# Kernel tuning notes

Hardware: AMD Instinct MI355X
Metric: run time of the kernel (lower is better)

Reference implementation:

```python
import jax, jax.numpy as jnp
import numpy as np

D_MODEL = 1024
L_MAX = 2048
BATCH = 4
ORDER = 2
FILTER_ORDER = 64
EMB_DIM = 3            # HyenaFilter default positional-embedding dim
SHORT_K = 3
HEAD_DIM = D_MODEL     # num_heads = 1
TOTAL_WIDTH = D_MODEL * (ORDER + 1)
# ExponentialModulation constants (Safari defaults)
MAX_DECAY = np.log(1e-2) / 0.3
MIN_DECAY = np.log(1e-2) / 1.5


def setup_inputs() -> dict:
    key = jax.random.key(0)
    ks = jax.random.split(key, 12)
    s = 0.02
    return {
        "u": jax.random.normal(ks[0], (BATCH, L_MAX, D_MODEL), jnp.float32),
        "in_w": jax.random.normal(ks[1], (D_MODEL, TOTAL_WIDTH), jnp.float32) * s,
        "in_b": jnp.zeros((TOTAL_WIDTH,), jnp.float32),
        "short_w": jax.random.normal(ks[2], (TOTAL_WIDTH, 1, SHORT_K), jnp.float32) * 0.3,
        "short_b": jnp.zeros((TOTAL_WIDTH,), jnp.float32),
        "mlp_w0": jax.random.normal(ks[3], (EMB_DIM, FILTER_ORDER), jnp.float32) * 0.4,
        "mlp_b0": jnp.zeros((FILTER_ORDER,), jnp.float32),
        "freq0": 10.0 * jnp.ones((1, FILTER_ORDER), jnp.float32),
        "mlp_w1": jax.random.normal(ks[4], (FILTER_ORDER, FILTER_ORDER), jnp.float32) * 0.12,
        "mlp_b1": jnp.zeros((FILTER_ORDER,), jnp.float32),
        "freq1": 10.0 * jnp.ones((1, FILTER_ORDER), jnp.float32),
        "mlp_w2": jax.random.normal(ks[5], (FILTER_ORDER, FILTER_ORDER), jnp.float32) * 0.12,
        "mlp_b2": jnp.zeros((FILTER_ORDER,), jnp.float32),
        "freq2": 10.0 * jnp.ones((1, FILTER_ORDER), jnp.float32),
        "mlp_w3": jax.random.normal(ks[6], (FILTER_ORDER, HEAD_DIM), jnp.float32) * 0.1,
        "filter_bias": jax.random.normal(ks[7], (HEAD_DIM,), jnp.float32),
        "out_w": jax.random.normal(ks[8], (D_MODEL, D_MODEL), jnp.float32) * s,
        "out_b": jnp.zeros((D_MODEL,), jnp.float32),
    }


def _pos_emb(L):
    # PositionalEmbedding: t in [0,1], plus exp(-1j * f * w) real/imag bands
    bands = (EMB_DIM - 1) // 2
    t = jnp.linspace(0.0, 1.0, L, dtype=jnp.float32)[:, None]                # (L, 1)
    w = 2.0 * jnp.pi * jnp.linspace(0.0, L - 1.0, L, dtype=jnp.float32)[:, None] / L
    f = jnp.linspace(1e-4, float(bands - 1), bands, dtype=jnp.float32)[None, :]
    phase = f * w                                                             # (L, bands)
    # exp(-1j*phase): real = cos(phase), imag = -sin(phase)
    z = jnp.concatenate([t, jnp.cos(phase), -jnp.sin(phase)], axis=-1)        # (L, EMB_DIM)
    return z, t


def _implicit_filter(L, mlp_w0, mlp_b0, freq0, mlp_w1, mlp_b1, freq1,
                     mlp_w2, mlp_b2, freq2, mlp_w3):
    z, t = _pos_emb(L)
    h = jnp.sin(freq0 * (z @ mlp_w0 + mlp_b0))
    h = jnp.sin(freq1 * (h @ mlp_w1 + mlp_b1))
    h = jnp.sin(freq2 * (h @ mlp_w2 + mlp_b2))
    h = h @ mlp_w3                                                            # (L, HEAD_DIM)
    # ExponentialModulation (shift = 0)
    deltas = jnp.linspace(MIN_DECAY, MAX_DECAY, HEAD_DIM, dtype=jnp.float32)[None, :]
    h = h * jnp.exp(-t * jnp.abs(deltas))
    return h                                                                  # (L, HEAD_DIM)


def _fftconv(u, k, bias):
    # u: (b, v, L), k: (v, L), bias: (v,) -- causal linear conv via 2L FFT
    L = u.shape[-1]
    n = 2 * L
    k_f = jnp.fft.rfft(k, n=n) / n                                            # (v, n//2+1)
    u_f = jnp.fft.rfft(u, n=n)                                                # (b, v, n//2+1)
    y = jnp.fft.irfft(u_f * k_f, n=n, norm="forward")[..., :L]
    return y + u * bias[:, None]


def reference(u, in_w, in_b, short_w, short_b,
              mlp_w0, mlp_b0, freq0, mlp_w1, mlp_b1, freq1,
              mlp_w2, mlp_b2, freq2, mlp_w3, filter_bias, out_w, out_b):
    b, l, d = u.shape
    up = u @ in_w + in_b                                                      # (b, l, 3d)
    up = jnp.transpose(up, (0, 2, 1))                                         # (b, 3d, l)
    # depthwise causal short conv (torch pad=k-1 both sides then [:l] == left pad only)
    uc = jax.lax.conv_general_dilated(
        up, short_w, window_strides=(1,), padding=[(SHORT_K - 1, 0)],
        dimension_numbers=("NCH", "OIH", "NCH"), feature_group_count=TOTAL_WIDTH)
    uc = uc + short_b[None, :, None]                                          # (b, 3d, l)
    x0, x1, v = jnp.split(uc, ORDER + 1, axis=1)                              # each (b, d, l)
    k = _implicit_filter(l, mlp_w0, mlp_b0, freq0, mlp_w1, mlp_b1, freq1,
                         mlp_w2, mlp_b2, freq2, mlp_w3).T                     # (d, l)
    v = v * x1                                                                # gate
    v = _fftconv(v, k, filter_bias)                                           # long conv
    y = jnp.transpose(v * x0, (0, 2, 1))                                      # (b, l, d)
    return y @ out_w + out_b
```

## Files before the change

kernel.cpp:

```cpp
#include <hip/hip_runtime.h>
#include <stdint.h>

typedef unsigned short u16;
typedef __attribute__((ext_vector_type(8))) short short8;
typedef __attribute__((ext_vector_type(4))) short short4x;
typedef __attribute__((ext_vector_type(4))) float f32x4;

#define PI_F 3.14159265358979323846f
#define L_SEQ 2048
#define NFFT 4096
#define DM 1024
#define TW 3072
#define BATCH 4

__device__ __forceinline__ u16 f2bf(float f){
  union { float f; uint32_t u; } v; v.f = f;
  uint32_t r = v.u + 0x7fffu + ((v.u >> 16) & 1u);
  return (u16)(r >> 16);
}
__device__ __forceinline__ float bf2f(u16 h){
  union { uint32_t u; float f; } v; v.u = ((uint32_t)h) << 16;
  return v.f;
}

__device__ __forceinline__ void async16(const void* g, void* l){
  __builtin_amdgcn_global_load_lds(
      (const __attribute__((address_space(1))) void*)g,
      (__attribute__((address_space(3))) void*)l, 16, 0, 0);
}

__device__ __forceinline__ void sincos_rev(float rev, float& sn, float& cs){
  asm("v_sin_f32 %0, %1" : "=v"(sn) : "v"(rev));
  asm("v_cos_f32 %0, %1" : "=v"(cs) : "v"(rev));
}

__device__ __forceinline__ float2 cmulf(float2 a, float c, float s){
  return make_float2(a.x*c - a.y*s, a.x*s + a.y*c);
}

__device__ __forceinline__ int P16(int i){ return i + (i >> 4); }

__device__ static constexpr int BR4[16] = {0,8,4,12,2,10,6,14,1,9,5,13,3,11,7,15};

template<int SGN>
__device__ __forceinline__ void fft16(float2* a){
  const float s = (float)SGN;
  static constexpr float tc[8]  = {1.f, 0.92387953f, 0.70710678f, 0.38268343f,
                                   0.f, -0.38268343f, -0.70710678f, -0.92387953f};
  static constexpr float ts_[8] = {0.f, -0.38268343f, -0.70710678f, -0.92387953f,
                                   -1.f, -0.92387953f, -0.70710678f, -0.38268343f};
  #pragma unroll
  for (int j = 0; j < 8; ++j){
    float2 u = a[j], v = a[j+8];
    float2 d = make_float2(u.x - v.x, u.y - v.y);
    a[j] = make_float2(u.x + v.x, u.y + v.y);
    a[j+8] = cmulf(d, tc[j], s*ts_[j]);
  }
  #pragma unroll
  for (int g = 0; g < 2; ++g){
    int b = g*8;
    #pragma unroll
    for (int j = 0; j < 4; ++j){
      float2 u = a[b+j], v = a[b+j+4];
      float2 d = make_float2(u.x - v.x, u.y - v.y);
      a[b+j] = make_float2(u.x + v.x, u.y + v.y);
      a[b+j+4] = cmulf(d, tc[2*j], s*ts_[2*j]);
    }
  }
  #pragma unroll
  for (int g = 0; g < 4; ++g){
    int b = g*4;
    #pragma unroll
    for (int j = 0; j < 2; ++j){
      float2 u = a[b+j], v = a[b+j+2];
      float2 d = make_float2(u.x - v.x, u.y - v.y);
      a[b+j] = make_float2(u.x + v.x, u.y + v.y);
      a[b+j+2] = (j == 0) ? d : cmulf(d, 0.f, -s);
    }
  }
  #pragma unroll
  for (int g = 0; g < 8; ++g){
    int b = g*2;
    float2 u = a[b], v = a[b+1];
    a[b] = make_float2(u.x + v.x, u.y + v.y);
    a[b+1] = make_float2(u.x - v.x, u.y - v.y);
  }
}

__global__ void k_convert_u(const float4* __restrict__ in, u16* __restrict__ outp, int n4){
  int idx = blockIdx.x * blockDim.x + threadIdx.x;
  int stride = gridDim.x * blockDim.x;
  for (int i = idx; i < n4; i += stride){
    float4 v = in[i];
    u16 r0 = f2bf(v.x), r1 = f2bf(v.y), r2 = f2bf(v.z), r3 = f2bf(v.w);
    u16* o = outp + (size_t)i * 4;
    o[0] = r0; o[1] = r1; o[2] = r2; o[3] = r3;
  }
}

__global__ void k_transpose_w(const float* __restrict__ in, u16* __restrict__ outp, int K, int N){
  __shared__ float tile[32][33];
  int n0 = blockIdx.x * 32, k0 = blockIdx.y * 32;
  int x = threadIdx.x, y = threadIdx.y;
  for (int i = 0; i < 4; ++i)
    tile[y + i*8][x] = in[(size_t)(k0 + y + i*8) * N + n0 + x];
  __syncthreads();
  for (int i = 0; i < 4; ++i)
    outp[(size_t)(n0 + y + i*8) * K + k0 + x] = f2bf(tile[x][y + i*8]);
}

__global__ void k_filter_h2(const float* __restrict__ w0, const float* __restrict__ b0, const float* __restrict__ f0,
                            const float* __restrict__ w1, const float* __restrict__ b1, const float* __restrict__ f1,
                            const float* __restrict__ w2, const float* __restrict__ b2, const float* __restrict__ f2,
                            float* __restrict__ H2T){
  int t = blockIdx.x;
  int j = threadIdx.x;
  float tn = t * (1.0f / 2047.0f);
  float ph = 1e-4f * 2.0f * PI_F * (float)t * (1.0f / 2048.0f);
  float z0 = tn, z1 = cosf(ph), z2 = -sinf(ph);
  __shared__ float hs[64];
  float pre = z0 * w0[j] + z1 * w0[64 + j] + z2 * w0[128 + j] + b0[j];
  float h = sinf(f0[j] * pre);
  hs[j] = h;
  __syncthreads();
  float acc = b1[j];
  for (int i = 0; i < 64; ++i) acc += hs[i] * w1[i*64 + j];
  h = sinf(f1[j] * acc);
  __syncthreads();
  hs[j] = h;
  __syncthreads();
  acc = b2[j];
  for (int i = 0; i < 64; ++i) acc += hs[i] * w2[i*64 + j];
  h = sinf(f2[j] * acc);
  H2T[j * L_SEQ + t] = h;
}

__global__ __launch_bounds__(256) void k_filter_fft16(const float* __restrict__ H2T,
                                                      const float* __restrict__ w3,
                                                      float2* __restrict__ Kf){
  int c0 = blockIdx.x * 2;
  int t = threadIdx.x;
  __shared__ float2 S[4352];
  __shared__ float wcol[2][64];
  if (t < 64){ wcol[0][t] = w3[t * DM + c0]; wcol[1][t] = w3[t * DM + c0 + 1]; }
  __syncthreads();
  const int n1 = t & 15, hi = t >> 4;
  float absd0 = 3.070113457325394f + 12.280453829301576f * ((float)c0 * (1.0f / 1023.0f));
  float absd1 = 3.070113457325394f + 12.280453829301576f * ((float)(c0+1) * (1.0f / 1023.0f));
  float sa[8] = {0,0,0,0,0,0,0,0}, sb[8] = {0,0,0,0,0,0,0,0};
  for (int j = 0; j < 64; ++j){
    float wa = wcol[0][j], wb = wcol[1][j];
    const float* hrow = H2T + j * L_SEQ + t;
    #pragma unroll
    for (int n3 = 0; n3 < 8; ++n3){
      float h = hrow[n3 << 8];
      sa[n3] += h * wa; sb[n3] += h * wb;
    }
  }
  float2 r[16];
  #pragma unroll
  for (int n3 = 0; n3 < 8; ++n3){
    int n = t + (n3 << 8);
    float tn = (float)n * (1.0f / 2047.0f);
    r[n3] = make_float2(sa[n3] * __expf(-tn * absd0), sb[n3] * __expf(-tn * absd1));
    r[n3 + 8] = make_float2(0.f, 0.f);
  }
  fft16<1>(r);
  #pragma unroll
  for (int k3 = 0; k3 < 16; ++k3){
    float sn, cs; sincos_rev(-(float)(hi * k3) * (1.0f/256.0f), sn, cs);
    S[P16(k3*256 + hi*16 + n1)] = cmulf(r[BR4[k3]], cs, sn);
  }
  __syncthreads();
  #pragma unroll
  for (int n2 = 0; n2 < 16; ++n2)
    r[n2] = S[P16(hi*256 + n2*16 + n1)];
  __syncthreads();
  fft16<1>(r);
  #pragma unroll
  for (int k2 = 0; k2 < 16; ++k2){
    float sn, cs; sincos_rev(-(float)(n1 * (hi + 16*k2)) * (1.0f/4096.0f), sn, cs);
    S[P16(k2*256 + hi*16 + n1)] = cmulf(r[BR4[k2]], cs, sn);
  }
  __syncthreads();
  #pragma unroll
  for (int m = 0; m < 16; ++m)
    r[m] = S[P16(hi*256 + n1*16 + m)];
  __syncthreads();
  fft16<1>(r);
  #pragma unroll
  for (int k1 = 0; k1 < 16; ++k1)
    S[P16(t + (k1 << 8))] = r[BR4[k1]];
  __syncthreads();
  const float inv = 1.0f / (float)NFFT;
  float2* kf0 = Kf + (size_t)c0 * NFFT;
  float2* kf1 = kf0 + NFFT;
  int mt = (256 - t) & 255;
  #pragma unroll
  for (int k1 = 0; k1 < 16; ++k1){
    int k = t + (k1 << 8);
    int mk1 = (t == 0) ? ((16 - k1) & 15) : (15 - k1);
    float2 Zk = r[BR4[k1]];
    float2 Zm = S[P16(mt + (mk1 << 8))];
    float gar = 0.5f*(Zk.x + Zm.x), gai = 0.5f*(Zk.y - Zm.y);
    float gbr = 0.5f*(Zk.y + Zm.y), gbi = 0.5f*(Zm.x - Zk.x);
    kf0[k] = make_float2(gar*inv, gai*inv);
    kf1[k] = make_float2(gbr*inv, gbi*inv);
  }
}

__device__ __forceinline__ void gbar(){ __builtin_amdgcn_s_barrier(); }
__device__ __forceinline__ void lgk0(){
  asm volatile("s_waitcnt lgkmcnt(0)" ::: "memory");
  __builtin_amdgcn_sched_barrier(0);
}
template<int V>
__device__ __forceinline__ void waitvm(){
  if constexpr (V == 8) asm volatile("s_waitcnt vmcnt(8)" ::: "memory");
  else if constexpr (V == 6) asm volatile("s_waitcnt vmcnt(6)" ::: "memory");
  else asm volatile("s_waitcnt vmcnt(0)" ::: "memory");
  __builtin_amdgcn_sched_barrier(0);
}

template<int BM, int BN, bool OUT_BF16>
__global__ __launch_bounds__(512, 2) void k_gemm8(const u16* __restrict__ A, const u16* __restrict__ Bt,
                                                  const float* __restrict__ bias, void* __restrict__ Cout,
                                                  int M, int N, int K){
  constexpr int MR  = BM / 32;
  constexpr int NR  = BN / 64;
  constexpr int LA  = BM / 128;
  constexpr int LB  = BN / 128;
  constexpr int V   = 2 * (LA + LB);
  static_assert(LA * 128 == BM && LB * 128 == BN, "stage divisors");
  __shared__ __align__(16) u16 lds[2 * 64 * (BM + BN)];
  const int tid = threadIdx.x;
  const int lane = tid & 63, w = tid >> 6;
  const int wm = w >> 2, wn = w & 3;
  const int lr = lane & 15, lk8 = (lane >> 4) * 8;
  const int NT = K >> 6;

  const int NNT = N / BN;
  int nwg = gridDim.x;
  int swz = (blockIdx.x & 7) * (nwg >> 3) + (blockIdx.x >> 3);
  int m0 = (swz / NNT) * BM;
  int n0 = (swz % NNT) * BN;

  u16* baseA = lds;
  u16* baseB = lds + 2 * 64 * BM;

  auto stageA = [&](int kts, int db, int kh){
    int kc0 = (kts << 6) + kh * 32;
    u16* slab = baseA + db * (BM * 64) + kh * (BM * 32);
    #pragma unroll
    for (int q = 0; q < LA; ++q){
      int row = q * 128 + (tid >> 2);
      int cl = ((tid & 3) * 8) ^ (((row >> 1) & 3) << 3);
      async16(A + (size_t)(m0 + row) * K + kc0 + cl, slab + q * 4096 + (w << 9));
    }
  };
  auto stageB = [&](int kts, int db, int kh){
    int kc0 = (kts << 6) + kh * 32;
    u16* slab = baseB + db * (BN * 64) + kh * (BN * 32);
    #pragma unroll
    for (int q = 0; q < LB; ++q){
      int row = q * 128 + (tid >> 2);
      int cl = ((tid & 3) * 8) ^ (((row >> 1) & 3) << 3);
      async16(Bt + (size_t)(n0 + row) * K + kc0 + cl, slab + q * 4096 + (w << 9));
    }
  };

  f32x4 acc[MR][NR] = {};
  short8 af[MR], bf[NR];

  auto readA = [&](int db, int kh){
    const u16* base = baseA + db * (BM * 64) + kh * (BM * 32);
    #pragma unroll
    for (int i = 0; i < MR; ++i){
      int ar = wm * (BM / 2) + i * 16 + lr;
      af[i] = *(const short8*)&base[ar * 32 + (lk8 ^ (((ar >> 1) & 3) << 3))];
    }
  };
  auto readB = [&](int db, int kh){
    const u16* base = baseB + db * (BN * 64) + kh * (BN * 32);
    #pragma unroll
    for (int j = 0; j < NR; ++j){
      int br = wn * (BN / 4) + j * 16 + lr;
      bf[j] = *(const short8*)&base[br * 32 + (lk8 ^ (((br >> 1) & 3) << 3))];
    }
  };

#define MFMA_FULL                                                              \
  __builtin_amdgcn_s_setprio(1);                                               \
  _Pragma("unroll")                                                            \
  for (int i = 0; i < MR; ++i)                                                 \
    _Pragma("unroll")                                                          \
    for (int j = 0; j < NR; ++j)                                               \
      acc[i][j] = __builtin_amdgcn_mfma_f32_16x16x32_bf16(                     \
          af[i], bf[j], acc[i][j], 0, 0, 0);                                   \
  __builtin_amdgcn_s_setprio(0);

  stageA(0, 0, 0); stageB(0, 0, 0);
  stageA(0, 0, 1); stageB(0, 0, 1);
  stageA(1, 1, 0); stageB(1, 1, 0);
  waitvm<V>();
  gbar();

  for (int kt = 0; kt < NT; ++kt){
    int b = kt & 1, bn2 = b ^ 1;
    int t1 = (kt + 1 < NT) ? kt + 1 : 0;
    int t2 = (kt + 2 < NT) ? kt + 2 : 0;
    readB(b, 0); readA(b, 0);
    stageA(t1, bn2, 1); stageB(t1, bn2, 1);
    gbar(); lgk0();
    MFMA_FULL
    waitvm<V>();
    gbar();
    readB(b, 1); readA(b, 1);
    stageA(t2, b, 0); stageB(t2, b, 0);
    gbar(); lgk0();
    MFMA_FULL
    waitvm<V>();
    gbar();
  }
#undef MFMA_FULL

  waitvm<0>();
  gbar();
  if constexpr (OUT_BF16){
    constexpr int BST = BN + 8;
    u16* lbuf = lds;
    #pragma unroll
    for (int j = 0; j < NR; ++j){
      int col = wn * (BN / 4) + j * 16 + lr;
      float bv = bias[n0 + col];
      #pragma unroll
      for (int i = 0; i < MR; ++i){
        int rw = wm * (BM / 2) + i * 16 + (lane >> 4) * 4;
        #pragma unroll
        for (int r = 0; r < 4; ++r)
          lbuf[(rw + r) * BST + col] = f2bf(acc[i][j][r] + bv);
      }
    }
    gbar();
    constexpr int ROWCH = BN / 8;
    constexpr int CHUNKS = BM * ROWCH;
    #pragma unroll
    for (int q = 0; q < CHUNKS / 512; ++q){
      int c = tid + q * 512;
      int row = c / ROWCH, col8 = (c % ROWCH) * 8;
      f32x4 vv = *(const f32x4*)&lbuf[row * BST + col8];
      *(f32x4*)((u16*)Cout + (size_t)(m0 + row) * N + n0 + col8) = vv;
    }
  } else {
    constexpr int BSTF = BN + 4;
    float* lbuf = (float*)lds;
    constexpr int ROWCHF = BN / 4;
    constexpr int CHUNKSF = (BM / 2) * ROWCHF;
    #pragma unroll
    for (int p = 0; p < 2; ++p){
      if (wm == p){
        #pragma unroll
        for (int j = 0; j < NR; ++j){
          int col = wn * (BN / 4) + j * 16 + lr;
          float bv = bias[n0 + col];
          #pragma unroll
          for (int i = 0; i < MR; ++i){
            int rl = i * 16 + (lane >> 4) * 4;
            #pragma unroll
            for (int r = 0; r < 4; ++r)
              lbuf[(rl + r) * BSTF + col] = acc[i][j][r] + bv;
          }
        }
      }
      gbar();
      #pragma unroll
      for (int q = 0; q < CHUNKSF / 512; ++q){
        int c = tid + q * 512;
        int row = c / ROWCHF, col4 = (c % ROWCHF) * 4;
        f32x4 vv = *(const f32x4*)&lbuf[row * BSTF + col4];
        *(f32x4*)((float*)Cout + (size_t)(m0 + p * (BM / 2) + row) * N + n0 + col4) = vv;
      }
      gbar();
    }
  }
}

__device__ __forceinline__ int ogcol(int c, int t){ return c * 136 + (t ^ (((c >> 3) & 7) << 4)); }

__global__ __launch_bounds__(256) void k_shortconv(const u16* __restrict__ up, const float* __restrict__ sw,
                            const float* __restrict__ sb,
                            u16* __restrict__ gOut, u16* __restrict__ x0Out){
  __shared__ u16 og[2][64 * 136];
  const int t0 = blockIdx.x * 128;
  const int c0 = blockIdx.y * 64;
  const int b  = blockIdx.z;
  const int tid = threadIdx.x;
  const int c8 = (tid & 7) * 8;
  const int tt = (tid >> 3) * 4;
  const int cg = c0 + c8;

  auto conv_group = [&](int g2, float out[8][4]){
    const f32x4* wp = (const f32x4*)(sw + (size_t)(g2 * DM + cg) * 3);
    f32x4 w03 = wp[0], w47 = wp[1], w8b = wp[2], wcf = wp[3], wgj = wp[4], wkn = wp[5];
    float wv[24];
    #pragma unroll
    for (int x = 0; x < 4; ++x){ wv[x] = w03[x]; wv[4+x] = w47[x]; wv[8+x] = w8b[x];
                                 wv[12+x] = wcf[x]; wv[16+x] = wgj[x]; wv[20+x] = wkn[x]; }
    const f32x4* bp = (const f32x4*)(sb + g2 * DM + cg);
    f32x4 b03 = bp[0], b47 = bp[1];
    float bv[8];
    #pragma unroll
    for (int x = 0; x < 4; ++x){ bv[x] = b03[x]; bv[4+x] = b47[x]; }
    const u16* base = up + ((size_t)(b * L_SEQ + t0 + tt - 2)) * TW + g2 * DM + cg;
    short8 rows[6];
    #pragma unroll
    for (int r = 0; r < 6; ++r){
      int t = t0 + tt - 2 + r;
      if (t >= 0) rows[r] = *(const short8*)(base + (size_t)r * TW);
      else rows[r] = (short8)0;
    }
    #pragma unroll
    for (int j = 0; j < 8; ++j){
      float w0 = wv[j*3], w1 = wv[j*3+1], w2 = wv[j*3+2], bb = bv[j];
      #pragma unroll
      for (int q = 0; q < 4; ++q){
        out[j][q] = w0 * bf2f((u16)rows[q][j]) + w1 * bf2f((u16)rows[q+1][j])
                  + w2 * bf2f((u16)rows[q+2][j]) + bb;
      }
    }
  };

  float x1v[8][4], gv[8][4], x0v[8][4];
  conv_group(1, x1v);
  conv_group(2, gv);
  #pragma unroll
  for (int j = 0; j < 8; ++j)
    #pragma unroll
    for (int q = 0; q < 4; ++q) gv[j][q] *= x1v[j][q];
  conv_group(0, x0v);

  #pragma unroll
  for (int j = 0; j < 8; ++j){
    short4x px, pg;
    #pragma unroll
    for (int q = 0; q < 4; ++q){ px[q] = (short)f2bf(x0v[j][q]); pg[q] = (short)f2bf(gv[j][q]); }
    int col = ogcol(c8 + j, tt);
    *(short4x*)&og[0][col] = px;
    *(short4x*)&og[1][col] = pg;
  }
  __syncthreads();

  #pragma unroll
  for (int q = 0; q < 4; ++q){
    int ch = tid + q * 256;
    int c = ch >> 4, t8 = (ch & 15) * 8;
    size_t gb = ((size_t)(b * DM + c0 + c)) * L_SEQ + t0 + t8;
    f32x4 v0 = *(const f32x4*)&og[0][ogcol(c, t8)];
    *(f32x4*)(x0Out + gb) = v0;
    f32x4 v1 = *(const f32x4*)&og[1][ogcol(c, t8)];
    *(f32x4*)(gOut + gb) = v1;
  }
}

__global__ __launch_bounds__(256) void k_fftconv(const u16* __restrict__ g, const u16* __restrict__ x0,
                          const float2* __restrict__ Kf, const float* __restrict__ fbias,
                          u16* __restrict__ z){
  int c0 = blockIdx.x * 2;
  int b = blockIdx.y;
  int t = threadIdx.x;
  __shared__ float2 S[4352];
  const size_t row0 = ((size_t)(b * DM + c0)) * L_SEQ;
  const size_t row1 = row0 + L_SEQ;
  const int n1 = t & 15, hi = t >> 4;
  float2 r[16];
  #pragma unroll
  for (int n3 = 0; n3 < 8; ++n3){
    int n = t + (n3 << 8);
    r[n3] = make_float2(bf2f(g[row0 + n]), bf2f(g[row1 + n]));
    r[n3 + 8] = make_float2(0.f, 0.f);
  }
  fft16<1>(r);
  #pragma unroll
  for (int k3 = 0; k3 < 16; ++k3){
    float sn, cs; sincos_rev(-(float)(hi * k3) * (1.0f/256.0f), sn, cs);
    S[P16(k3*256 + hi*16 + n1)] = cmulf(r[BR4[k3]], cs, sn);
  }
  __syncthreads();
  #pragma unroll
  for (int n2 = 0; n2 < 16; ++n2)
    r[n2] = S[P16(hi*256 + n2*16 + n1)];
  __syncthreads();
  fft16<1>(r);
  #pragma unroll
  for (int k2 = 0; k2 < 16; ++k2){
    float sn, cs; sincos_rev(-(float)(n1 * (hi + 16*k2)) * (1.0f/4096.0f), sn, cs);
    S[P16(k2*256 + hi*16 + n1)] = cmulf(r[BR4[k2]], cs, sn);
  }
  __syncthreads();
  #pragma unroll
  for (int m = 0; m < 16; ++m)
    r[m] = S[P16(hi*256 + n1*16 + m)];
  __syncthreads();
  fft16<1>(r);
  #pragma unroll
  for (int k1 = 0; k1 < 16; ++k1)
    S[P16(t + (k1 << 8))] = r[BR4[k1]];
  __syncthreads();
  const float2* kf0 = Kf + (size_t)c0 * NFFT;
  const float2* kf1 = kf0 + NFFT;
  int mt = (256 - t) & 255;
  float2 y[16];
  #pragma unroll
  for (int k1 = 0; k1 < 16; ++k1){
    int k = t + (k1 << 8);
    int mk1 = (t == 0) ? ((16 - k1) & 15) : (15 - k1);
    float2 Zk = r[BR4[k1]];
    float2 Zm = S[P16(mt + (mk1 << 8))];
    float2 K0 = kf0[k], K1 = kf1[k];
    float gar = 0.5f*(Zk.x + Zm.x), gai = 0.5f*(Zk.y - Zm.y);
    float gbr = 0.5f*(Zk.y + Zm.y), gbi = 0.5f*(Zm.x - Zk.x);
    float yar = gar*K0.x - gai*K0.y, yai = gar*K0.y + gai*K0.x;
    float ybr = gbr*K1.x - gbi*K1.y, ybi = gbr*K1.y + gbi*K1.x;
    y[k1] = make_float2(yar - ybi, yai + ybr);
  }
  fft16<-1>(y);
  __syncthreads();
  #pragma unroll
  for (int n3 = 0; n3 < 16; ++n3){
    float sn, cs; sincos_rev((float)(hi * n3) * (1.0f/256.0f), sn, cs);
    S[P16(n3*256 + hi*16 + n1)] = cmulf(y[BR4[n3]], cs, sn);
  }
  __syncthreads();
  #pragma unroll
  for (int m2 = 0; m2 < 16; ++m2)
    r[m2] = S[P16(hi*256 + m2*16 + n1)];
  __syncthreads();
  fft16<-1>(r);
  #pragma unroll
  for (int nn2 = 0; nn2 < 16; ++nn2){
    float sn, cs; sincos_rev((float)(n1 * (hi + 16*nn2)) * (1.0f/4096.0f), sn, cs);
    S[P16(nn2*256 + hi*16 + n1)] = cmulf(r[BR4[nn2]], cs, sn);
  }
  __syncthreads();
  #pragma unroll
  for (int m = 0; m < 16; ++m)
    r[m] = S[P16(hi*256 + n1*16 + m)];
  fft16<-1>(r);
  float fb0 = fbias[c0], fb1 = fbias[c0+1];
  #pragma unroll
  for (int q = 0; q < 8; ++q){
    int n = t + (q << 8);
    float2 val = r[BR4[q]];
    float g0 = bf2f(g[row0 + n]), g1 = bf2f(g[row1 + n]);
    float x00 = bf2f(x0[row0 + n]), x01 = bf2f(x0[row1 + n]);
    z[row0 + n] = f2bf((val.x + g0*fb0) * x00);
    z[row1 + n] = f2bf((val.y + g1*fb1) * x01);
  }
}

__global__ void k_transpose_z(const u16* __restrict__ zin, u16* __restrict__ zout){
  __shared__ u16 tile[32][33];
  int l0 = blockIdx.x * 32, d0 = blockIdx.y * 32, b = blockIdx.z;
  int x = threadIdx.x, y = threadIdx.y;
  for (int i = 0; i < 4; ++i){
    int d = d0 + y + i*8;
    tile[y + i*8][x] = zin[((size_t)(b * DM + d)) * L_SEQ + l0 + x];
  }
  __syncthreads();
  for (int i = 0; i < 4; ++i){
    int l = l0 + y + i*8;
    zout[((size_t)(b * L_SEQ + l)) * DM + d0 + x] = tile[x][y + i*8];
  }
}

extern "C" void kernel_launch(void* const* d_in, const int* in_sizes, int n_in,
                              void* d_out, int out_size, void* d_ws, size_t ws_size,
                              hipStream_t stream){
  (void)in_sizes; (void)n_in; (void)out_size; (void)ws_size;
  const float* u       = (const float*)d_in[0];
  const float* in_w    = (const float*)d_in[1];
  const float* in_b    = (const float*)d_in[2];
  const float* short_w = (const float*)d_in[3];
  const float* short_b = (const float*)d_in[4];
  const float* w0 = (const float*)d_in[5];
  const float* b0 = (const float*)d_in[6];
  const float* f0 = (const float*)d_in[7];
  const float* w1 = (const float*)d_in[8];
  const float* b1 = (const float*)d_in[9];
  const float* f1 = (const float*)d_in[10];
  const float* w2 = (const float*)d_in[11];
  const float* b2 = (const float*)d_in[12];
  const float* f2 = (const float*)d_in[13];
  const float* w3 = (const float*)d_in[14];
  const float* fbias = (const float*)d_in[15];
  const float* out_w = (const float*)d_in[16];
  const float* out_b = (const float*)d_in[17];
  float* out = (float*)d_out;

  char* ws = (char*)d_ws;
  size_t off = 0;
  auto alloc = [&](size_t bytes)->void*{
    void* p = ws + off; off += (bytes + 255) & ~(size_t)255; return p;
  };
  const int M = BATCH * L_SEQ;
  u16*   u_bf  = (u16*)  alloc((size_t)M * DM * 2);
  u16*   inwT  = (u16*)  alloc((size_t)TW * DM * 2);
  u16*   outwT = (u16*)  alloc((size_t)DM * DM * 2);
  float* H2T   = (float*)alloc((size_t)L_SEQ * 64 * 4);
  float2* Kf   = (float2*)alloc((size_t)DM * NFFT * 8);
  u16*   up    = (u16*)  alloc((size_t)M * TW * 2);
  u16*   gbuf  = (u16*)  alloc((size_t)BATCH * DM * L_SEQ * 2);
  u16*   x0buf = (u16*)  alloc((size_t)BATCH * DM * L_SEQ * 2);
  u16*   z  = u_bf;
  u16*   zT = up;

  k_convert_u<<<2048, 256, 0, stream>>>((const float4*)u, u_bf, (M * DM) / 4);
  k_transpose_w<<<dim3(TW/32, DM/32), dim3(32, 8), 0, stream>>>(in_w, inwT, DM, TW);
  k_transpose_w<<<dim3(DM/32, DM/32), dim3(32, 8), 0, stream>>>(out_w, outwT, DM, DM);
  k_filter_h2<<<L_SEQ, 64, 0, stream>>>(w0, b0, f0, w1, b1, f1, w2, b2, f2, H2T);
  k_filter_fft16<<<DM/2, 256, 0, stream>>>(H2T, w3, Kf);
  k_gemm8<128, 384, true><<<dim3((M/128)*(TW/384)), 512, 0, stream>>>(u_bf, inwT, in_b, up, M, TW, DM);
  k_shortconv<<<dim3(L_SEQ/128, DM/64, BATCH), 256, 0, stream>>>(up, short_w, short_b, gbuf, x0buf);
  k_fftconv<<<dim3(DM/2, BATCH), 256, 0, stream>>>(gbuf, x0buf, Kf, fbias, z);
  k_transpose_z<<<dim3(L_SEQ/32, DM/32, BATCH), dim3(32, 8), 0, stream>>>(z, zT);
  k_gemm8<256, 128, false><<<dim3((M/256)*(DM/128)), 512, 0, stream>>>(zT, outwT, out_b, out, M, DM, DM);
}
```

Baseline: 191.2 us.

## Triple-buffer GEMM K-tiles with one barrier per iteration and retile both GEMMs

Replaces the double-buffered, half-K staging pipeline in the bf16 MFMA GEMM with a triple-buffered scheme. Each step issues loads for the full 64-wide K tile two steps ahead, waits only on the oldest tile, reads both K-halves into registers and runs all MFMAs between a single pair of barriers. Both the input projection and the output projection GEMMs now use 128x256 tiles. The aim is fewer barriers and deeper prefetch to hide global latency, at the cost of more LDS (one block per CU) and a changed grid and tile balance.

```diff
diff --git a/kernel.cpp b/kernel.cpp
--- a/kernel.cpp
+++ b/kernel.cpp
@@ -216,8 +216,7 @@
 }
 template<int V>
 __device__ __forceinline__ void waitvm(){
-  if constexpr (V == 8) asm volatile("s_waitcnt vmcnt(8)" ::: "memory");
-  else if constexpr (V == 6) asm volatile("s_waitcnt vmcnt(6)" ::: "memory");
+  if constexpr (V == 12) asm volatile("s_waitcnt vmcnt(12)" ::: "memory");
   else asm volatile("s_waitcnt vmcnt(0)" ::: "memory");
   __builtin_amdgcn_sched_barrier(0);
 }
@@ -230,9 +229,8 @@
   constexpr int NR  = BN / 64;
   constexpr int LA  = BM / 128;
   constexpr int LB  = BN / 128;
-  constexpr int V   = 2 * (LA + LB);
   static_assert(LA * 128 == BM && LB * 128 == BN, "stage divisors");
-  __shared__ __align__(16) u16 lds[2 * 64 * (BM + BN)];
+  __shared__ __align__(16) u16 lds[3 * 64 * (BM + BN)];
   const int tid = threadIdx.x;
   const int lane = tid & 63, w = tid >> 6;
   const int wm = w >> 2, wn = w & 3;
@@ -246,83 +244,68 @@
   int n0 = (swz % NNT) * BN;
 
   u16* baseA = lds;
-  u16* baseB = lds + 2 * 64 * BM;
-
-  auto stageA = [&](int kts, int db, int kh){
-    int kc0 = (kts << 6) + kh * 32;
-    u16* slab = baseA + db * (BM * 64) + kh * (BM * 32);
-    #pragma unroll
-    for (int q = 0; q < LA; ++q){
-      int row = q * 128 + (tid >> 2);
-      int cl = ((tid & 3) * 8) ^ (((row >> 1) & 3) << 3);
-      async16(A + (size_t)(m0 + row) * K + kc0 + cl, slab + q * 4096 + (w << 9));
+  u16* baseB = lds + 3 * 64 * BM;
+
+  auto stageTile = [&](int kts, int db){
+    #pragma unroll
+    for (int kh = 0; kh < 2; ++kh){
+      int kc0 = (kts << 6) + kh * 32;
+      u16* slabA = baseA + db * (BM * 64) + kh * (BM * 32);
+      #pragma unroll
+      for (int q = 0; q < LA; ++q){
+        int row = q * 128 + (tid >> 2);
+        int cl = ((tid & 3) * 8) ^ (((row >> 1) & 3) << 3);
+        async16(A + (size_t)(m0 + row) * K + kc0 + cl, slabA + q * 4096 + (w << 9));
+      }
+      u16* slabB = baseB + db * (BN * 64) + kh * (BN * 32);
+      #pragma unroll
+      for (int q = 0; q < LB; ++q){
+        int row = q * 128 + (tid >> 2);
+        int cl = ((tid & 3) * 8) ^ (((row >> 1) & 3) << 3);
+        async16(Bt + (size_t)(n0 + row) * K + kc0 + cl, slabB + q * 4096 + (w << 9));
+      }
     }
   };
-  auto stageB = [&](int kts, int db, int kh){
-    int kc0 = (kts << 6) + kh * 32;
-    u16* slab = baseB + db * (BN * 64) + kh * (BN * 32);
-    #pragma unroll
-    for (int q = 0; q < LB; ++q){
-      int row = q * 128 + (tid >> 2);
-      int cl = ((tid & 3) * 8) ^ (((row >> 1) & 3) << 3);
-      async16(Bt + (size_t)(n0 + row) * K + kc0 + cl, slab + q * 4096 + (w << 9));
-    }
-  };
 
   f32x4 acc[MR][NR] = {};
-  short8 af[MR], bf[NR];
-
-  auto readA = [&](int db, int kh){
-    const u16* base = baseA + db * (BM * 64) + kh * (BM * 32);
-    #pragma unroll
-    for (int i = 0; i < MR; ++i){
-      int ar = wm * (BM / 2) + i * 16 + lr;
-      af[i] = *(const short8*)&base[ar * 32 + (lk8 ^ (((ar >> 1) & 3) << 3))];
-    }
-  };
-  auto readB = [&](int db, int kh){
-    const u16* base = baseB + db * (BN * 64) + kh * (BN * 32);
-    #pragma unroll
-    for (int j = 0; j < NR; ++j){
-      int br = wn * (BN / 4) + j * 16 + lr;
-      bf[j] = *(const short8*)&base[br * 32 + (lk8 ^ (((br >> 1) & 3) << 3))];
-    }
-  };
-
-#define MFMA_FULL                                                              \
-  __builtin_amdgcn_s_setprio(1);                                               \
-  _Pragma("unroll")                                                            \
-  for (int i = 0; i < MR; ++i)                                                 \
-    _Pragma("unroll")                                                          \
-    for (int j = 0; j < NR; ++j)                                               \
-      acc[i][j] = __builtin_amdgcn_mfma_f32_16x16x32_bf16(                     \
-          af[i], bf[j], acc[i][j], 0, 0, 0);                                   \
-  __builtin_amdgcn_s_setprio(0);
-
-  stageA(0, 0, 0); stageB(0, 0, 0);
-  stageA(0, 0, 1); stageB(0, 0, 1);
-  stageA(1, 1, 0); stageB(1, 1, 0);
-  waitvm<V>();
-  gbar();
+  short8 af[2][MR], bf[2][NR];
+
+  stageTile(0, 0);
+  stageTile(1, 1);
 
   for (int kt = 0; kt < NT; ++kt){
-    int b = kt & 1, bn2 = b ^ 1;
-    int t1 = (kt + 1 < NT) ? kt + 1 : 0;
-    int t2 = (kt + 2 < NT) ? kt + 2 : 0;
-    readB(b, 0); readA(b, 0);
-    stageA(t1, bn2, 1); stageB(t1, bn2, 1);
-    gbar(); lgk0();
-    MFMA_FULL
-    waitvm<V>();
+    int db = kt % 3;
+    int kts = (kt + 2 < NT) ? kt + 2 : (kt + 2 - NT);
+    stageTile(kts, (kt + 2) % 3);
+    waitvm<12>();
     gbar();
-    readB(b, 1); readA(b, 1);
-    stageA(t2, b, 0); stageB(t2, b, 0);
-    gbar(); lgk0();
-    MFMA_FULL
-    waitvm<V>();
+    #pragma unroll
+    for (int h = 0; h < 2; ++h){
+      const u16* bA = baseA + db * (BM * 64) + h * (BM * 32);
+      #pragma unroll
+      for (int i = 0; i < MR; ++i){
+        int ar = wm * (BM / 2) + i * 16 + lr;
+        af[h][i] = *(const short8*)&bA[ar * 32 + (lk8 ^ (((ar >> 1) & 3) << 3))];
+      }
+      const u16* bB = baseB + db * (BN * 64) + h * (BN * 32);
+      #pragma unroll
+      for (int j = 0; j < NR; ++j){
+        int br = wn * (BN / 4) + j * 16 + lr;
+        bf[h][j] = *(const short8*)&bB[br * 32 + (lk8 ^ (((br >> 1) & 3) << 3))];
+      }
+    }
+    lgk0();
+    __builtin_amdgcn_s_setprio(1);
+    #pragma unroll
+    for (int h = 0; h < 2; ++h)
+      #pragma unroll
+      for (int i = 0; i < MR; ++i)
+        #pragma unroll
+        for (int j = 0; j < NR; ++j)
+          acc[i][j] = __builtin_amdgcn_mfma_f32_16x16x32_bf16(af[h][i], bf[h][j], acc[i][j], 0, 0, 0);
+    __builtin_amdgcn_s_setprio(0);
     gbar();
   }
-#undef MFMA_FULL
 
   waitvm<0>();
   gbar();
@@ -619,9 +602,9 @@
   k_transpose_w<<<dim3(DM/32, DM/32), dim3(32, 8), 0, stream>>>(out_w, outwT, DM, DM);
   k_filter_h2<<<L_SEQ, 64, 0, stream>>>(w0, b0, f0, w1, b1, f1, w2, b2, f2, H2T);
   k_filter_fft16<<<DM/2, 256, 0, stream>>>(H2T, w3, Kf);
-  k_gemm8<128, 384, true><<<dim3((M/128)*(TW/384)), 512, 0, stream>>>(u_bf, inwT, in_b, up, M, TW, DM);
+  k_gemm8<128, 256, true><<<dim3((M/128)*(TW/256)), 512, 0, stream>>>(u_bf, inwT, in_b, up, M, TW, DM);
   k_shortconv<<<dim3(L_SEQ/128, DM/64, BATCH), 256, 0, stream>>>(up, short_w, short_b, gbuf, x0buf);
   k_fftconv<<<dim3(DM/2, BATCH), 256, 0, stream>>>(gbuf, x0buf, Kf, fbias, z);
   k_transpose_z<<<dim3(L_SEQ/32, DM/32, BATCH), dim3(32, 8), 0, stream>>>(z, zT);
-  k_gemm8<256, 128, false><<<dim3((M/256)*(DM/128)), 512, 0, stream>>>(zT, outwT, out_b, out, M, DM, DM);
-}
+  k_gemm8<128, 256, false><<<dim3((M/128)*(DM/256)), 512, 0, stream>>>(zT, outwT, out_b, out, M, DM, DM);
+}
```

Measured after the change: 196.0 us. 1.03x slower.

## Loop over batch inside fftconv block and precompute twiddles once

Applied to the files above, without the earlier changes.

The fftconv kernel now launches one block per channel pair and loops over the four batch entries inside, instead of one block per (channel pair, batch). Twiddle factors are computed once into registers and reused for forward and inverse passes across all batches, and the filter spectrum loads stay within the block for possible cache reuse. This cuts repeated sincos work, but the grid shrinks from 2048 to 512 blocks, which lowers parallelism on a large GPU. The 64 extra twiddle registers also add register pressure.

```diff
diff --git a/kernel.cpp b/kernel.cpp
--- a/kernel.cpp
+++ b/kernel.cpp
@@ -466,95 +466,96 @@
                           const float2* __restrict__ Kf, const float* __restrict__ fbias,
                           u16* __restrict__ z){
   int c0 = blockIdx.x * 2;
-  int b = blockIdx.y;
   int t = threadIdx.x;
   __shared__ float2 S[4352];
-  const size_t row0 = ((size_t)(b * DM + c0)) * L_SEQ;
-  const size_t row1 = row0 + L_SEQ;
   const int n1 = t & 15, hi = t >> 4;
-  float2 r[16];
-  #pragma unroll
-  for (int n3 = 0; n3 < 8; ++n3){
-    int n = t + (n3 << 8);
-    r[n3] = make_float2(bf2f(g[row0 + n]), bf2f(g[row1 + n]));
-    r[n3 + 8] = make_float2(0.f, 0.f);
-  }
-  fft16<1>(r);
-  #pragma unroll
-  for (int k3 = 0; k3 < 16; ++k3){
-    float sn, cs; sincos_rev(-(float)(hi * k3) * (1.0f/256.0f), sn, cs);
-    S[P16(k3*256 + hi*16 + n1)] = cmulf(r[BR4[k3]], cs, sn);
-  }
-  __syncthreads();
-  #pragma unroll
-  for (int n2 = 0; n2 < 16; ++n2)
-    r[n2] = S[P16(hi*256 + n2*16 + n1)];
-  __syncthreads();
-  fft16<1>(r);
-  #pragma unroll
-  for (int k2 = 0; k2 < 16; ++k2){
-    float sn, cs; sincos_rev(-(float)(n1 * (hi + 16*k2)) * (1.0f/4096.0f), sn, cs);
-    S[P16(k2*256 + hi*16 + n1)] = cmulf(r[BR4[k2]], cs, sn);
-  }
-  __syncthreads();
-  #pragma unroll
-  for (int m = 0; m < 16; ++m)
-    r[m] = S[P16(hi*256 + n1*16 + m)];
-  __syncthreads();
-  fft16<1>(r);
-  #pragma unroll
-  for (int k1 = 0; k1 < 16; ++k1)
-    S[P16(t + (k1 << 8))] = r[BR4[k1]];
-  __syncthreads();
+  float t1c[16], t1s[16], t2c[16], t2s[16];
+  #pragma unroll
+  for (int k = 0; k < 16; ++k){
+    sincos_rev(-(float)(hi * k) * (1.0f/256.0f), t1s[k], t1c[k]);
+    sincos_rev(-(float)(n1 * (hi + 16*k)) * (1.0f/4096.0f), t2s[k], t2c[k]);
+  }
   const float2* kf0 = Kf + (size_t)c0 * NFFT;
   const float2* kf1 = kf0 + NFFT;
-  int mt = (256 - t) & 255;
-  float2 y[16];
-  #pragma unroll
-  for (int k1 = 0; k1 < 16; ++k1){
-    int k = t + (k1 << 8);
-    int mk1 = (t == 0) ? ((16 - k1) & 15) : (15 - k1);
-    float2 Zk = r[BR4[k1]];
-    float2 Zm = S[P16(mt + (mk1 << 8))];
-    float2 K0 = kf0[k], K1 = kf1[k];
-    float gar = 0.5f*(Zk.x + Zm.x), gai = 0.5f*(Zk.y - Zm.y);
-    float gbr = 0.5f*(Zk.y + Zm.y), gbi = 0.5f*(Zm.x - Zk.x);
-    float yar = gar*K0.x - gai*K0.y, yai = gar*K0.y + gai*K0.x;
-    float ybr = gbr*K1.x - gbi*K1.y, ybi = gbr*K1.y + gbi*K1.x;
-    y[k1] = make_float2(yar - ybi, yai + ybr);
-  }
-  fft16<-1>(y);
-  __syncthreads();
-  #pragma unroll
-  for (int n3 = 0; n3 < 16; ++n3){
-    float sn, cs; sincos_rev((float)(hi * n3) * (1.0f/256.0f), sn, cs);
-    S[P16(n3*256 + hi*16 + n1)] = cmulf(y[BR4[n3]], cs, sn);
-  }
-  __syncthreads();
-  #pragma unroll
-  for (int m2 = 0; m2 < 16; ++m2)
-    r[m2] = S[P16(hi*256 + m2*16 + n1)];
-  __syncthreads();
-  fft16<-1>(r);
-  #pragma unroll
-  for (int nn2 = 0; nn2 < 16; ++nn2){
-    float sn, cs; sincos_rev((float)(n1 * (hi + 16*nn2)) * (1.0f/4096.0f), sn, cs);
-    S[P16(nn2*256 + hi*16 + n1)] = cmulf(r[BR4[nn2]], cs, sn);
-  }
-  __syncthreads();
-  #pragma unroll
-  for (int m = 0; m < 16; ++m)
-    r[m] = S[P16(hi*256 + n1*16 + m)];
-  fft16<-1>(r);
-  float fb0 = fbias[c0], fb1 = fbias[c0+1];
-  #pragma unroll
-  for (int q = 0; q < 8; ++q){
-    int n = t + (q << 8);
-    float2 val = r[BR4[q]];
-    float g0 = bf2f(g[row0 + n]), g1 = bf2f(g[row1 + n]);
-    float x00 = bf2f(x0[row0 + n]), x01 = bf2f(x0[row1 + n]);
-    z[row0 + n] = f2bf((val.x + g0*fb0) * x00);
-    z[row1 + n] = f2bf((val.y + g1*fb1) * x01);
+  const float fb0 = fbias[c0], fb1 = fbias[c0+1];
+  const int mt = (256 - t) & 255;
+
+  for (int b = 0; b < BATCH; ++b){
+    const size_t row0 = ((size_t)(b * DM + c0)) * L_SEQ;
+    const size_t row1 = row0 + L_SEQ;
+    float2 r[16];
+    #pragma unroll
+    for (int n3 = 0; n3 < 8; ++n3){
+      int n = t + (n3 << 8);
+      r[n3] = make_float2(bf2f(g[row0 + n]), bf2f(g[row1 + n]));
+      r[n3 + 8] = make_float2(0.f, 0.f);
+    }
+    fft16<1>(r);
+    __syncthreads();
+    #pragma unroll
+    for (int k3 = 0; k3 < 16; ++k3)
+      S[P16(k3*256 + hi*16 + n1)] = cmulf(r[BR4[k3]], t1c[k3], t1s[k3]);
+    __syncthreads();
+    #pragma unroll
+    for (int n2 = 0; n2 < 16; ++n2)
+      r[n2] = S[P16(hi*256 + n2*16 + n1)];
+    __syncthreads();
+    fft16<1>(r);
+    #pragma unroll
+    for (int k2 = 0; k2 < 16; ++k2)
+      S[P16(k2*256 + hi*16 + n1)] = cmulf(r[BR4[k2]], t2c[k2], t2s[k2]);
+    __syncthreads();
+    #pragma unroll
+    for (int m = 0; m < 16; ++m)
+      r[m] = S[P16(hi*256 + n1*16 + m)];
+    __syncthreads();
+    fft16<1>(r);
+    #pragma unroll
+    for (int k1 = 0; k1 < 16; ++k1)
+      S[P16(t + (k1 << 8))] = r[BR4[k1]];
+    __syncthreads();
+    float2 y[16];
+    #pragma unroll
+    for (int k1 = 0; k1 < 16; ++k1){
+      int k = t + (k1 << 8);
+      int mk1 = (t == 0) ? ((16 - k1) & 15) : (15 - k1);
+      float2 Zk = r[BR4[k1]];
+      float2 Zm = S[P16(mt + (mk1 << 8))];
+      float2 K0 = kf0[k], K1 = kf1[k];
+      float gar = 0.5f*(Zk.x + Zm.x), gai = 0.5f*(Zk.y - Zm.y);
+      float gbr = 0.5f*(Zk.y + Zm.y), gbi = 0.5f*(Zm.x - Zk.x);
+      float yar = gar*K0.x - gai*K0.y, yai = gar*K0.y + gai*K0.x;
+      float ybr = gbr*K1.x - gbi*K1.y, ybi = gbr*K1.y + gbi*K1.x;
+      y[k1] = make_float2(yar - ybi, yai + ybr);
+    }
+    fft16<-1>(y);
+    __syncthreads();
+    #pragma unroll
+    for (int n3 = 0; n3 < 16; ++n3)
+      S[P16(n3*256 + hi*16 + n1)] = cmulf(y[BR4[n3]], t1c[n3], -t1s[n3]);
+    __syncthreads();
+    #pragma unroll
+    for (int m2 = 0; m2 < 16; ++m2)
+      r[m2] = S[P16(hi*256 + m2*16 + n1)];
+    __syncthreads();
+    fft16<-1>(r);
+    #pragma unroll
+    for (int nn2 = 0; nn2 < 16; ++nn2)
+      S[P16(nn2*256 + hi*16 + n1)] = cmulf(r[BR4[nn2]], t2c[nn2], -t2s[nn2]);
+    __syncthreads();
+    #pragma unroll
+    for (int m = 0; m < 16; ++m)
+      r[m] = S[P16(hi*256 + n1*16 + m)];
+    fft16<-1>(r);
+    #pragma unroll
+    for (int q = 0; q < 8; ++q){
+      int n = t + (q << 8);
+      float2 val = r[BR4[q]];
+      float g0 = bf2f(g[row0 + n]), g1 = bf2f(g[row1 + n]);
+      float x00 = bf2f(x0[row0 + n]), x01 = bf2f(x0[row1 + n]);
+      z[row0 + n] = f2bf((val.x + g0*fb0) * x00);
+      z[row1 + n] = f2bf((val.y + g1*fb1) * x01);
+    }
   }
 }
 
@@ -621,7 +622,7 @@
   k_filter_fft16<<<DM/2, 256, 0, stream>>>(H2T, w3, Kf);
   k_gemm8<128, 384, true><<<dim3((M/128)*(TW/384)), 512, 0, stream>>>(u_bf, inwT, in_b, up, M, TW, DM);
   k_shortconv<<<dim3(L_SEQ/128, DM/64, BATCH), 256, 0, stream>>>(up, short_w, short_b, gbuf, x0buf);
-  k_fftconv<<<dim3(DM/2, BATCH), 256, 0, stream>>>(gbuf, x0buf, Kf, fbias, z);
+  k_fftconv<<<dim3(DM/2), 256, 0, stream>>>(gbuf, x0buf, Kf, fbias, z);
   k_transpose_z<<<dim3(L_SEQ/32, DM/32, BATCH), dim3(32, 8), 0, stream>>>(z, zT);
   k_gemm8<256, 128, false><<<dim3((M/256)*(DM/128)), 512, 0, stream>>>(zT, outwT, out_b, out, M, DM, DM);
 }
```

Result: slower. 237.1 us (+24.0%).
